# Performance work log

Measured on AMD Instinct MI355X. Metric: run time of the kernel, lower is better.

## Reference

```python
import jax, jax.numpy as jnp
import numpy as np

# Dims: B=16 graphs, T=354 timesteps (l_max), N=64 nodes, H=128 model dim, NS=32 complex SSM modes

def setup_inputs() -> dict:
    key = jax.random.key(0)
    ks = jax.random.split(key, 10)
    B, T, N, H, NS = 16, 354, 64, 128, 32
    x = jax.random.normal(ks[0], (B, T, N), jnp.float32)
    W_in = jax.random.normal(ks[1], (H, 1), jnp.float32) * 0.5
    b_in = jnp.zeros((H,), jnp.float32)
    # S4D params: timescales log-uniform in [1e-3, 1e-1], A = -1/2 + i*pi*n (S4D-Lin init)
    log_dt = (jnp.log(0.001) + jax.random.uniform(ks[2], (H,), jnp.float32) * (jnp.log(0.1) - jnp.log(0.001))).astype(jnp.float32)
    A_re = -0.5 * jnp.ones((H, NS), jnp.float32)
    A_im = jnp.broadcast_to(np.pi * jnp.arange(NS, dtype=jnp.float32), (H, NS)).astype(jnp.float32) + 0.0
    C_re = jax.random.normal(ks[3], (H, NS), jnp.float32) * (0.5 ** 0.5)
    C_im = jax.random.normal(ks[4], (H, NS), jnp.float32) * (0.5 ** 0.5)
    D = jax.random.normal(ks[5], (H,), jnp.float32)
    W_out = jax.random.normal(ks[6], (2 * H, H), jnp.float32) * (1.0 / np.sqrt(H))
    b_out = jnp.zeros((2 * H,), jnp.float32)
    W_cls = jax.random.normal(ks[7], (1, H), jnp.float32) * (1.0 / np.sqrt(H))
    b_cls = jnp.zeros((1,), jnp.float32)
    return {"x": x, "W_in": W_in, "b_in": b_in, "log_dt": log_dt, "A_re": A_re, "A_im": A_im,
            "C_re": C_re, "C_im": C_im, "D": D, "W_out": W_out, "b_out": b_out,
            "W_cls": W_cls, "b_cls": b_cls}


def reference(x, W_in, b_in, log_dt, A_re, A_im, C_re, C_im, D, W_out, b_out, W_cls, b_cls):
    B, T, N = x.shape
    H = W_in.shape[0]
    # (B,T,N) -> (B*N, T, 1) per-node scalar series
    u = x.transpose(0, 2, 1).reshape(B * N, T, 1)
    u = u * W_in[:, 0] + b_in            # input_proj: (BN, T, H)
    u = u.transpose(0, 2, 1)             # transposed layout: (BN, H, L)
    # ---- S4D kernel (ZOH discretization, conjugate-pair 2*Re trick) ----
    dt = jnp.exp(log_dt)                 # (H,)
    A = A_re + 1j * A_im                 # (H, NS) complex64
    dtA = A * dt[:, None]                # (H, NS)
    C = C_re + 1j * C_im
    C_disc = C * (jnp.exp(dtA) - 1.0) / A
    l = jnp.arange(T)
    vand = jnp.exp(dtA[:, :, None] * l)  # Vandermonde (H, NS, L)
    K = 2.0 * jnp.real(jnp.einsum('hn,hnl->hl', C_disc, vand))  # (H, L)
    # ---- FFT causal long convolution + skip ----
    n_fft = 2 * T
    yf = jnp.fft.rfft(u, n_fft) * jnp.fft.rfft(K, n_fft)
    y = jnp.fft.irfft(yf, n_fft)[..., :T] + D[:, None] * u   # (BN, H, L)
    y = jax.nn.gelu(y)
    # dropout: identity at inference
    # ---- position-wise output linear H -> 2H, then GLU over channels ----
    g = jnp.einsum('bhl,gh->bgl', y, W_out) + b_out[:, None]  # (BN, 2H, L)
    z = g[:, :H] * jax.nn.sigmoid(g[:, H:])                    # (BN, H, L)
    # ---- pooling + classifier ----
    node_feats = z.mean(axis=-1).reshape(B, N, H)
    graph_feats = node_feats.mean(axis=1)                      # (B, H)
    logits = graph_feats @ W_cls.T + b_cls                     # (B, 1)
    return logits
```

## Files before the change

### kernel.cpp

```cpp
#include <hip/hip_runtime.h>
#include <hip/hip_bf16.h>


#define B_  16
#define T_  354
#define N_  64
#define H_  128
#define NS_ 32
#define BN_ (B_*N_)
#define TP_ 384
#define KW_ 512
#define PAD_ 136
#define GC_ 4
#define NGC_ ((T_ + GC_ - 1) / GC_)
#define GT_ 16
#define NGT_ ((T_ + GT_ - 1) / GT_)
#define WB_ ((2 * H_ * H_) / 512)

typedef __attribute__((ext_vector_type(8))) short bf16x8;
typedef __attribute__((ext_vector_type(4))) float f32x4;

static __device__ __forceinline__ unsigned short f32_to_bf16(float f) {
    unsigned int u = __float_as_uint(f);
    unsigned int r = 0x7FFFu + ((u >> 16) & 1u);
    return (unsigned short)((u + r) >> 16);
}

static __device__ __forceinline__ void gload_lds4(const void* g, void* l) {
    __builtin_amdgcn_global_load_lds(
        (const __attribute__((address_space(1))) unsigned int*)g,
        (__attribute__((address_space(3))) unsigned int*)l, 4, 0, 0);
}

static __device__ __forceinline__ float gelu_f(float v) {
    float v2 = v * v;
    float x  = v * fmaf(0.0713548162726f, v2, 1.5957691216057f);
    float sg = 1.0f / (1.0f + __expf(-x));
    return v * sg;
}

__global__ __launch_bounds__(512) void k_pre(
        const float* __restrict__ log_dt,
        const float* __restrict__ A_re, const float* __restrict__ A_im,
        const float* __restrict__ C_re, const float* __restrict__ C_im,
        const float* __restrict__ b_in, const float* __restrict__ D,
        const float* __restrict__ x, const float* __restrict__ W_out,
        unsigned short* __restrict__ Krev, float* __restrict__ koff,
        unsigned short* __restrict__ xbf, unsigned short* __restrict__ Wbf) {
    const int blk = blockIdx.x;
    const int tid = threadIdx.x;

    if (blk >= H_ + 96) {
        int id = (blk - H_ - 96) * 512 + tid;
        if (id < 2 * H_ * H_) Wbf[id] = f32_to_bf16(W_out[id]);
        return;
    }
    if (blk >= H_) {
        __shared__ float xt[64][68];
        int idx = blk - H_;
        int bt = idx / 6, tt = idx % 6;
        int r  = tid >> 3, fc = tid & 7;
        int t  = tt * 64 + r;
        float4 v0 = make_float4(0.f, 0.f, 0.f, 0.f), v1 = v0;
        if (t < T_) {
            const float* xp = x + ((size_t)bt * T_ + t) * N_ + fc * 8;
            v0 = *(const float4*)xp;
            v1 = *(const float4*)(xp + 4);
        }
        *(float4*)&xt[r][fc * 8]     = v0;
        *(float4*)&xt[r][fc * 8 + 4] = v1;
        __syncthreads();
        int n = tid >> 3, tc = tid & 7;
        unsigned short pk[8];
#pragma unroll
        for (int k = 0; k < 8; k++) pk[k] = f32_to_bf16(xt[tc * 8 + k][n]);
        *(uint4*)(xbf + (size_t)(bt * 64 + n) * TP_ + tt * 64 + tc * 8)
            = *(const uint4*)pk;
        return;
    }

    const int h = blk;
    const int l = tid;
    float val = 0.0f;
    if (l < T_) {
        float dt = expf(log_dt[h]);
        float fl = (float)l;
#pragma unroll 4
        for (int m = 0; m < NS_; m++) {
            float are = A_re[h * NS_ + m], aim = A_im[h * NS_ + m];
            float dre = are * dt, dim = aim * dt;
            float er  = expf(dre);
            float c1, s1; __sincosf(dim, &s1, &c1);
            float e_re = er * c1, e_im = er * s1;
            float m_re = e_re - 1.0f, m_im = e_im;
            float inv  = 1.0f / (are * are + aim * aim);
            float q_re = (m_re * are + m_im * aim) * inv;
            float q_im = (m_im * are - m_re * aim) * inv;
            float c_r = C_re[h * NS_ + m], c_i = C_im[h * NS_ + m];
            float cdre = c_r * q_re - c_i * q_im;
            float cdim = c_r * q_im + c_i * q_re;
            float el = expf(dre * fl);
            float cl, sl; __sincosf(dim * fl, &sl, &cl);
            val += el * (cdre * cl - cdim * sl);
        }
        val *= 2.0f;
        if (l == 0) val += D[h];
    }

    __shared__ float sc[512];
    sc[l] = (l < T_) ? val : 0.0f;
    __syncthreads();
    for (int off = 1; off < 512; off <<= 1) {
        float add = (l >= off) ? sc[l - off] : 0.0f;
        __syncthreads();
        sc[l] += add;
        __syncthreads();
    }

    if (l < T_) {
        koff[l * H_ + h] = b_in[h] * sc[l];
        unsigned short bv = f32_to_bf16(val);
#pragma unroll
        for (int r = 0; r < 8; r++)
            Krev[((size_t)r * H_ + h) * KW_ + (T_ - 1 - l) + r] = bv;
    }
}

__global__ __launch_bounds__(256, 3) void k_conv(
        const unsigned short* __restrict__ xbf,
        const unsigned short* __restrict__ Krev,
        const float* __restrict__ koff,
        const float* __restrict__ W_in,
        unsigned short* __restrict__ Y) {
    __shared__ unsigned short x_lds[64 * PAD_];
    __shared__ unsigned short k_lds[128 * PAD_];

    const int tid  = threadIdx.x;
    const int w    = tid >> 6;
    const int lane = tid & 63;
    const int q    = lane >> 4;
    const int l16  = lane & 15;
    const int bn0  = blockIdx.x * 64;
    const int tg0  = blockIdx.y * GC_;

    float win[2][4];
#pragma unroll
    for (int mt = 0; mt < 2; mt++)
#pragma unroll
        for (int rr = 0; rr < 4; rr++)
            win[mt][rr] = W_in[32 * w + 16 * mt + 4 * q + rr];

    for (int g = 0; g < GC_; g++) {
        const int t = tg0 + g;
        if (t >= T_) break;
        const int nkb = (t >> 7) + 1;

        float ko[2][4];
#pragma unroll
        for (int mt = 0; mt < 2; mt++)
#pragma unroll
            for (int rr = 0; rr < 4; rr++)
                ko[mt][rr] = koff[t * H_ + 32 * w + 16 * mt + 4 * q + rr];

        f32x4 cacc[2][4];
#pragma unroll
        for (int mt = 0; mt < 2; mt++)
#pragma unroll
            for (int nt = 0; nt < 4; nt++) cacc[mt][nt] = (f32x4){0.f, 0.f, 0.f, 0.f};

        for (int kb = 0; kb < nkb; kb++) {
            const int tau0 = kb << 7;
            const int L    = 353 - t + tau0;
            const int cp   = (-L) & 7;
            const int kshi = min(3, (t - tau0) >> 5);
            __syncthreads();
#pragma unroll
            for (int i = 0; i < 16; i++) {
                int r = w * 16 + i;
                gload_lds4(xbf + (size_t)(bn0 + r) * TP_ + tau0 + lane * 2,
                           &x_lds[r * PAD_]);
            }
#pragma unroll 8
            for (int i = 0; i < 32; i++) {
                int hr = w * 32 + i;
                gload_lds4(Krev + ((size_t)cp * H_ + hr) * KW_ + (L + cp) + lane * 2,
                           &k_lds[hr * PAD_]);
            }
            __syncthreads();

            for (int ks = 0; ks <= kshi; ks++) {
                bf16x8 af[2], bf[4];
#pragma unroll
                for (int mt = 0; mt < 2; mt++)
                    af[mt] = *(const bf16x8*)&k_lds[(32 * w + 16 * mt + l16) * PAD_ + ks * 32 + q * 8];
#pragma unroll
                for (int nt = 0; nt < 4; nt++)
                    bf[nt] = *(const bf16x8*)&x_lds[(16 * nt + l16) * PAD_ + ks * 32 + q * 8];
#pragma unroll
                for (int mt = 0; mt < 2; mt++)
#pragma unroll
                    for (int nt = 0; nt < 4; nt++)
                        cacc[mt][nt] = __builtin_amdgcn_mfma_f32_16x16x32_bf16(
                            af[mt], bf[nt], cacc[mt][nt], 0, 0, 0);
            }
        }

        __syncthreads();
#pragma unroll
        for (int mt = 0; mt < 2; mt++)
#pragma unroll
            for (int nt = 0; nt < 4; nt++) {
                unsigned short pk[4];
#pragma unroll
                for (int rr = 0; rr < 4; rr++) {
                    float v = fmaf(cacc[mt][nt][rr], win[mt][rr], ko[mt][rr]);
                    pk[rr] = f32_to_bf16(gelu_f(v));
                }
                *(uint2*)&x_lds[(16 * nt + l16) * PAD_ + 32 * w + 16 * mt + 4 * q]
                    = *(const uint2*)pk;
            }
        __syncthreads();

#pragma unroll
        for (int i = 0; i < 4; i++) {
            int c    = i * 256 + tid;
            int row  = c >> 4;
            int col8 = (c & 15) * 8;
            uint4 v = *(const uint4*)&x_lds[row * PAD_ + col8];
            *(uint4*)(Y + ((size_t)t * BN_ + bn0 + row) * H_ + col8) = v;
        }
    }
}

__global__ __launch_bounds__(256, 4) void k_glu(
        const unsigned short* __restrict__ Y,
        const unsigned short* __restrict__ Wbf,
        const float* __restrict__ b_out,
        float* __restrict__ node_sum) {
    __shared__ unsigned short Yt[64 * PAD_];

    const int tid  = threadIdx.x;
    const int w    = tid >> 6;
    const int lane = tid & 63;
    const int q    = lane >> 4;
    const int l16  = lane & 15;
    const int jg   = blockIdx.x & 1;
    const int bn0  = (blockIdx.x >> 1) * 64;
    const int tg0  = blockIdx.y * GT_;
    const int jlow = jg * 64 + w * 16;
    const int jhigh = jlow + 128;

    bf16x8 wfrag[2][4];
#pragma unroll
    for (int ks = 0; ks < 4; ks++) {
        wfrag[0][ks] = *(const bf16x8*)(Wbf + (size_t)(jlow  + l16) * H_ + ks * 32 + q * 8);
        wfrag[1][ks] = *(const bf16x8*)(Wbf + (size_t)(jhigh + l16) * H_ + ks * 32 + q * 8);
    }
    float bo1[4], bo2[4];
#pragma unroll
    for (int rr = 0; rr < 4; rr++) {
        bo1[rr] = b_out[jlow  + 4 * q + rr];
        bo2[rr] = b_out[jhigh + 4 * q + rr];
    }

    f32x4 zacc[4];
#pragma unroll
    for (int nt = 0; nt < 4; nt++) zacc[nt] = (f32x4){0.f, 0.f, 0.f, 0.f};

    for (int g = 0; g < GT_; g++) {
        const int t = tg0 + g;
        if (t >= T_) break;
        __syncthreads();
#pragma unroll
        for (int i = 0; i < 16; i++) {
            int r = w * 16 + i;
            gload_lds4(Y + ((size_t)t * BN_ + bn0 + r) * H_ + lane * 2,
                       &Yt[r * PAD_]);
        }
        __syncthreads();

        f32x4 gacc[2][4];
#pragma unroll
        for (int mt = 0; mt < 2; mt++)
#pragma unroll
            for (int nt = 0; nt < 4; nt++) gacc[mt][nt] = (f32x4){0.f, 0.f, 0.f, 0.f};

#pragma unroll
        for (int ks = 0; ks < 4; ks++) {
            bf16x8 yf[4];
#pragma unroll
            for (int nt = 0; nt < 4; nt++)
                yf[nt] = *(const bf16x8*)&Yt[(16 * nt + l16) * PAD_ + ks * 32 + q * 8];
#pragma unroll
            for (int mt = 0; mt < 2; mt++)
#pragma unroll
                for (int nt = 0; nt < 4; nt++)
                    gacc[mt][nt] = __builtin_amdgcn_mfma_f32_16x16x32_bf16(
                        wfrag[mt][ks], yf[nt], gacc[mt][nt], 0, 0, 0);
        }

#pragma unroll
        for (int nt = 0; nt < 4; nt++)
#pragma unroll
            for (int rr = 0; rr < 4; rr++) {
                float a  = gacc[0][nt][rr] + bo1[rr];
                float bs = gacc[1][nt][rr] + bo2[rr];
                float sg = 1.0f / (1.0f + __expf(-bs));
                zacc[nt][rr] += a * sg;
            }
    }

#pragma unroll
    for (int nt = 0; nt < 4; nt++)
#pragma unroll
        for (int rr = 0; rr < 4; rr++) {
            int bn = bn0 + 16 * nt + l16;
            int j  = jlow + 4 * q + rr;
            atomicAdd(&node_sum[bn * H_ + j], zacc[nt][rr]);
        }
}

__global__ void k_cls(const float* __restrict__ node_sum,
                      const float* __restrict__ W_cls, const float* __restrict__ b_cls,
                      float* __restrict__ out) {
    const int b = blockIdx.x, tid = threadIdx.x;
    float s = 0.0f;
    for (int i = tid; i < N_ * H_; i += 256)
        s += node_sum[b * (N_ * H_) + i] * W_cls[i & (H_ - 1)];
    __shared__ float red[256];
    red[tid] = s;
    __syncthreads();
    for (int off = 128; off > 0; off >>= 1) {
        if (tid < off) red[tid] += red[tid + off];
        __syncthreads();
    }
    if (tid == 0) out[b] = red[0] * (1.0f / (354.0f * 64.0f)) + b_cls[0];
}

extern "C" void kernel_launch(void* const* d_in, const int* in_sizes, int n_in,
                              void* d_out, int out_size, void* d_ws, size_t ws_size,
                              hipStream_t stream) {
    const float* x      = (const float*)d_in[0];
    const float* W_in   = (const float*)d_in[1];
    const float* b_in   = (const float*)d_in[2];
    const float* log_dt = (const float*)d_in[3];
    const float* A_re   = (const float*)d_in[4];
    const float* A_im   = (const float*)d_in[5];
    const float* C_re   = (const float*)d_in[6];
    const float* C_im   = (const float*)d_in[7];
    const float* D      = (const float*)d_in[8];
    const float* W_out  = (const float*)d_in[9];
    const float* b_out  = (const float*)d_in[10];
    const float* W_cls  = (const float*)d_in[11];
    const float* b_cls  = (const float*)d_in[12];

    char* ws = (char*)d_ws;
    float*          node_sum = (float*)(ws + 0);
    unsigned short* Krev     = (unsigned short*)(ws + 524288);
    float*          koff     = (float*)(ws + 1572864);
    unsigned short* xbf      = (unsigned short*)(ws + 1754112);
    unsigned short* Wbf      = (unsigned short*)(ws + 2540544);
    unsigned short* Y        = (unsigned short*)(ws + 2606080);

    hipMemsetAsync(ws, 0, 1572864, stream);
    k_pre<<<dim3(H_ + 96 + WB_), dim3(512), 0, stream>>>(
        log_dt, A_re, A_im, C_re, C_im, b_in, D, x, W_out, Krev, koff, xbf, Wbf);
    k_conv<<<dim3(BN_ / 64, NGC_), dim3(256), 0, stream>>>(
        xbf, Krev, koff, W_in, Y);
    k_glu<<<dim3(2 * BN_ / 64, NGT_), dim3(256), 0, stream>>>(
        Y, Wbf, b_out, node_sum);
    k_cls<<<dim3(B_), dim3(256), 0, stream>>>(node_sum, W_cls, b_cls, (float*)d_out);
}
```

Baseline: 243.9 us.

## Register-prefetch software pipelining in conv and GLU kernels, halve GLU time grouping

Replaces the direct global-to-LDS loads in k_conv and k_glu with 16-byte register loads that prefetch the next tile while the current one is computed, then store it into LDS. k_glu gets a double-buffered LDS tile, and its time-group size drops from 16 to 8, giving more blocks. k_conv now writes its GELU outputs straight to global memory instead of staging them through LDS for coalescing. This aims to hide global load latency behind MFMA work. In exchange it raises register pressure, makes the Y stores less coalesced, and adds more atomic adds in k_glu because there are more blocks.

```diff
diff --git a/kernel.cpp b/kernel.cpp
--- a/kernel.cpp
+++ b/kernel.cpp
@@ -13,7 +13,7 @@
 #define PAD_ 136
 #define GC_ 4
 #define NGC_ ((T_ + GC_ - 1) / GC_)
-#define GT_ 16
+#define GT_ 8
 #define NGT_ ((T_ + GT_ - 1) / GT_)
 #define WB_ ((2 * H_ * H_) / 512)
 
@@ -24,12 +24,6 @@
     unsigned int u = __float_as_uint(f);
     unsigned int r = 0x7FFFu + ((u >> 16) & 1u);
     return (unsigned short)((u + r) >> 16);
-}
-
-static __device__ __forceinline__ void gload_lds4(const void* g, void* l) {
-    __builtin_amdgcn_global_load_lds(
-        (const __attribute__((address_space(1))) unsigned int*)g,
-        (__attribute__((address_space(3))) unsigned int*)l, 4, 0, 0);
 }
 
 static __device__ __forceinline__ float gelu_f(float v) {
@@ -135,13 +129,15 @@
     __shared__ unsigned short x_lds[64 * PAD_];
     __shared__ unsigned short k_lds[128 * PAD_];
 
-    const int tid  = threadIdx.x;
-    const int w    = tid >> 6;
-    const int lane = tid & 63;
-    const int q    = lane >> 4;
-    const int l16  = lane & 15;
-    const int bn0  = blockIdx.x * 64;
-    const int tg0  = blockIdx.y * GC_;
+    const int tid   = threadIdx.x;
+    const int w     = tid >> 6;
+    const int lane  = tid & 63;
+    const int q     = lane >> 4;
+    const int l16   = lane & 15;
+    const int bn0   = blockIdx.x * 64;
+    const int tg0   = blockIdx.y * GC_;
+    const int srow4 = lane >> 4;
+    const int scol  = l16 * 8;
 
     float win[2][4];
 #pragma unroll
@@ -150,85 +146,95 @@
         for (int rr = 0; rr < 4; rr++)
             win[mt][rr] = W_in[32 * w + 16 * mt + 4 * q + rr];
 
-    for (int g = 0; g < GC_; g++) {
-        const int t = tg0 + g;
-        if (t >= T_) break;
-        const int nkb = (t >> 7) + 1;
-
-        float ko[2][4];
-#pragma unroll
-        for (int mt = 0; mt < 2; mt++)
-#pragma unroll
-            for (int rr = 0; rr < 4; rr++)
-                ko[mt][rr] = koff[t * H_ + 32 * w + 16 * mt + 4 * q + rr];
-
-        f32x4 cacc[2][4];
-#pragma unroll
-        for (int mt = 0; mt < 2; mt++)
-#pragma unroll
-            for (int nt = 0; nt < 4; nt++) cacc[mt][nt] = (f32x4){0.f, 0.f, 0.f, 0.f};
-
-        for (int kb = 0; kb < nkb; kb++) {
-            const int tau0 = kb << 7;
-            const int L    = 353 - t + tau0;
-            const int cp   = (-L) & 7;
-            const int kshi = min(3, (t - tau0) >> 5);
-            __syncthreads();
-#pragma unroll
-            for (int i = 0; i < 16; i++) {
-                int r = w * 16 + i;
-                gload_lds4(xbf + (size_t)(bn0 + r) * TP_ + tau0 + lane * 2,
-                           &x_lds[r * PAD_]);
+    uint4 xr[4], kr[8];
+
+    auto LOAD = [&](int t, int kb) {
+        const int tau0 = kb << 7;
+        const int L    = 353 - t + tau0;
+        const int cp   = (-L) & 7;
+        const unsigned short* kbase = Krev + (size_t)cp * H_ * KW_ + (L + cp);
+#pragma unroll
+        for (int i = 0; i < 4; i++) {
+            int r = w * 16 + i * 4 + srow4;
+            xr[i] = *(const uint4*)(xbf + (size_t)(bn0 + r) * TP_ + tau0 + scol);
+        }
+#pragma unroll
+        for (int i = 0; i < 8; i++) {
+            int hr = w * 32 + i * 4 + srow4;
+            kr[i] = *(const uint4*)(kbase + (size_t)hr * KW_ + scol);
+        }
+    };
+    auto WRITE = [&]() {
+#pragma unroll
+        for (int i = 0; i < 4; i++) {
+            int r = w * 16 + i * 4 + srow4;
+            *(uint4*)&x_lds[r * PAD_ + scol] = xr[i];
+        }
+#pragma unroll
+        for (int i = 0; i < 8; i++) {
+            int hr = w * 32 + i * 4 + srow4;
+            *(uint4*)&k_lds[hr * PAD_ + scol] = kr[i];
+        }
+    };
+
+    f32x4 cacc[2][4];
+#pragma unroll
+    for (int mt = 0; mt < 2; mt++)
+#pragma unroll
+        for (int nt = 0; nt < 4; nt++) cacc[mt][nt] = (f32x4){0.f, 0.f, 0.f, 0.f};
+
+    int t = tg0, kb = 0;
+    bool valid = true;
+    LOAD(t, kb);
+    while (valid) {
+        int tn = t, kbn = kb + 1;
+        if (kbn > (t >> 7)) { tn = t + 1; kbn = 0; }
+        bool vn = (tn < T_) && (tn < tg0 + GC_);
+
+        __syncthreads();
+        WRITE();
+        if (vn) LOAD(tn, kbn);
+        __syncthreads();
+
+        const int tau0 = kb << 7;
+        const int kshi = min(3, (t - tau0) >> 5);
+        for (int ks = 0; ks <= kshi; ks++) {
+            bf16x8 af[2], bf[4];
+#pragma unroll
+            for (int mt = 0; mt < 2; mt++)
+                af[mt] = *(const bf16x8*)&k_lds[(32 * w + 16 * mt + l16) * PAD_ + ks * 32 + q * 8];
+#pragma unroll
+            for (int nt = 0; nt < 4; nt++)
+                bf[nt] = *(const bf16x8*)&x_lds[(16 * nt + l16) * PAD_ + ks * 32 + q * 8];
+#pragma unroll
+            for (int mt = 0; mt < 2; mt++)
+#pragma unroll
+                for (int nt = 0; nt < 4; nt++)
+                    cacc[mt][nt] = __builtin_amdgcn_mfma_f32_16x16x32_bf16(
+                        af[mt], bf[nt], cacc[mt][nt], 0, 0, 0);
+        }
+
+        if (kb == (t >> 7)) {
+#pragma unroll
+            for (int mt = 0; mt < 2; mt++) {
+                int h0 = 32 * w + 16 * mt + 4 * q;
+#pragma unroll
+                for (int nt = 0; nt < 4; nt++) {
+                    unsigned short pk[4];
+#pragma unroll
+                    for (int rr = 0; rr < 4; rr++) {
+                        float v = fmaf(cacc[mt][nt][rr], win[mt][rr],
+                                       koff[t * H_ + h0 + rr]);
+                        pk[rr] = f32_to_bf16(gelu_f(v));
+                    }
+                    int bn = bn0 + 16 * nt + l16;
+                    *(uint2*)(Y + ((size_t)t * BN_ + bn) * H_ + h0)
+                        = *(const uint2*)pk;
+                    cacc[mt][nt] = (f32x4){0.f, 0.f, 0.f, 0.f};
+                }
             }
-#pragma unroll 8
-            for (int i = 0; i < 32; i++) {
-                int hr = w * 32 + i;
-                gload_lds4(Krev + ((size_t)cp * H_ + hr) * KW_ + (L + cp) + lane * 2,
-                           &k_lds[hr * PAD_]);
-            }
-            __syncthreads();
-
-            for (int ks = 0; ks <= kshi; ks++) {
-                bf16x8 af[2], bf[4];
-#pragma unroll
-                for (int mt = 0; mt < 2; mt++)
-                    af[mt] = *(const bf16x8*)&k_lds[(32 * w + 16 * mt + l16) * PAD_ + ks * 32 + q * 8];
-#pragma unroll
-                for (int nt = 0; nt < 4; nt++)
-                    bf[nt] = *(const bf16x8*)&x_lds[(16 * nt + l16) * PAD_ + ks * 32 + q * 8];
-#pragma unroll
-                for (int mt = 0; mt < 2; mt++)
-#pragma unroll
-                    for (int nt = 0; nt < 4; nt++)
-                        cacc[mt][nt] = __builtin_amdgcn_mfma_f32_16x16x32_bf16(
-                            af[mt], bf[nt], cacc[mt][nt], 0, 0, 0);
-            }
-        }
-
-        __syncthreads();
-#pragma unroll
-        for (int mt = 0; mt < 2; mt++)
-#pragma unroll
-            for (int nt = 0; nt < 4; nt++) {
-                unsigned short pk[4];
-#pragma unroll
-                for (int rr = 0; rr < 4; rr++) {
-                    float v = fmaf(cacc[mt][nt][rr], win[mt][rr], ko[mt][rr]);
-                    pk[rr] = f32_to_bf16(gelu_f(v));
-                }
-                *(uint2*)&x_lds[(16 * nt + l16) * PAD_ + 32 * w + 16 * mt + 4 * q]
-                    = *(const uint2*)pk;
-            }
-        __syncthreads();
-
-#pragma unroll
-        for (int i = 0; i < 4; i++) {
-            int c    = i * 256 + tid;
-            int row  = c >> 4;
-            int col8 = (c & 15) * 8;
-            uint4 v = *(const uint4*)&x_lds[row * PAD_ + col8];
-            *(uint4*)(Y + ((size_t)t * BN_ + bn0 + row) * H_ + col8) = v;
-        }
+        }
+        t = tn; kb = kbn; valid = vn;
     }
 }
 
@@ -237,18 +243,20 @@
         const unsigned short* __restrict__ Wbf,
         const float* __restrict__ b_out,
         float* __restrict__ node_sum) {
-    __shared__ unsigned short Yt[64 * PAD_];
-
-    const int tid  = threadIdx.x;
-    const int w    = tid >> 6;
-    const int lane = tid & 63;
-    const int q    = lane >> 4;
-    const int l16  = lane & 15;
-    const int jg   = blockIdx.x & 1;
-    const int bn0  = (blockIdx.x >> 1) * 64;
-    const int tg0  = blockIdx.y * GT_;
-    const int jlow = jg * 64 + w * 16;
+    __shared__ unsigned short Yt[2][64 * PAD_];
+
+    const int tid   = threadIdx.x;
+    const int w     = tid >> 6;
+    const int lane  = tid & 63;
+    const int q     = lane >> 4;
+    const int l16   = lane & 15;
+    const int jg    = blockIdx.x & 1;
+    const int bn0   = (blockIdx.x >> 1) * 64;
+    const int tg0   = blockIdx.y * GT_;
+    const int jlow  = jg * 64 + w * 16;
     const int jhigh = jlow + 128;
+    const int srow4 = lane >> 4;
+    const int scol  = l16 * 8;
 
     bf16x8 wfrag[2][4];
 #pragma unroll
@@ -263,21 +271,35 @@
         bo2[rr] = b_out[jhigh + 4 * q + rr];
     }
 
+    uint4 pre[4];
+    auto LOADT = [&](int t) {
+#pragma unroll
+        for (int i = 0; i < 4; i++) {
+            int r = w * 16 + i * 4 + srow4;
+            pre[i] = *(const uint4*)(Y + ((size_t)t * BN_ + bn0 + r) * H_ + scol);
+        }
+    };
+    auto WRITEB = [&](int b) {
+#pragma unroll
+        for (int i = 0; i < 4; i++) {
+            int r = w * 16 + i * 4 + srow4;
+            *(uint4*)&Yt[b][r * PAD_ + scol] = pre[i];
+        }
+    };
+
     f32x4 zacc[4];
 #pragma unroll
     for (int nt = 0; nt < 4; nt++) zacc[nt] = (f32x4){0.f, 0.f, 0.f, 0.f};
+
+    LOADT(tg0);
+    WRITEB(0);
+    __syncthreads();
 
     for (int g = 0; g < GT_; g++) {
         const int t = tg0 + g;
         if (t >= T_) break;
-        __syncthreads();
-#pragma unroll
-        for (int i = 0; i < 16; i++) {
-            int r = w * 16 + i;
-            gload_lds4(Y + ((size_t)t * BN_ + bn0 + r) * H_ + lane * 2,
-                       &Yt[r * PAD_]);
-        }
-        __syncthreads();
+        const bool hn = (g + 1 < GT_) && (t + 1 < T_);
+        if (hn) LOADT(t + 1);
 
         f32x4 gacc[2][4];
 #pragma unroll
@@ -285,12 +307,13 @@
 #pragma unroll
             for (int nt = 0; nt < 4; nt++) gacc[mt][nt] = (f32x4){0.f, 0.f, 0.f, 0.f};
 
+        const unsigned short* buf = Yt[g & 1];
 #pragma unroll
         for (int ks = 0; ks < 4; ks++) {
             bf16x8 yf[4];
 #pragma unroll
             for (int nt = 0; nt < 4; nt++)
-                yf[nt] = *(const bf16x8*)&Yt[(16 * nt + l16) * PAD_ + ks * 32 + q * 8];
+                yf[nt] = *(const bf16x8*)&buf[(16 * nt + l16) * PAD_ + ks * 32 + q * 8];
 #pragma unroll
             for (int mt = 0; mt < 2; mt++)
 #pragma unroll
@@ -308,6 +331,9 @@
                 float sg = 1.0f / (1.0f + __expf(-bs));
                 zacc[nt][rr] += a * sg;
             }
+
+        if (hn) WRITEB((g + 1) & 1);
+        __syncthreads();
     }
 
 #pragma unroll
```

New measurement: 406.5 us. 66.7% more time.

## Compute two timesteps per conv block sharing x tiles, load K directly to registers

Applied to the files above, without the earlier changes.

The conv kernel now handles two adjacent output timesteps per block, so each loaded x tile in LDS feeds both timesteps' MFMAs. The K operand is read straight from global memory into registers instead of being staged through a separate LDS buffer, which frees LDS and removes that copy. The causal k-substep skipping (kshi) is dropped, so each active block step runs all four k-substeps. The grid grows to T/2 blocks in y, and the GLU kernel's time tile shrinks from 16 to 8. Costs are more accumulator registers and uncoalesced-per-lane global loads for K.

```diff
diff --git a/kernel.cpp b/kernel.cpp
--- a/kernel.cpp
+++ b/kernel.cpp
@@ -11,9 +11,7 @@
 #define TP_ 384
 #define KW_ 512
 #define PAD_ 136
-#define GC_ 4
-#define NGC_ ((T_ + GC_ - 1) / GC_)
-#define GT_ 16
+#define GT_ 8
 #define NGT_ ((T_ + GT_ - 1) / GT_)
 #define WB_ ((2 * H_ * H_) / 512)
 
@@ -133,7 +131,6 @@
         const float* __restrict__ W_in,
         unsigned short* __restrict__ Y) {
     __shared__ unsigned short x_lds[64 * PAD_];
-    __shared__ unsigned short k_lds[128 * PAD_];
 
     const int tid  = threadIdx.x;
     const int w    = tid >> 6;
@@ -141,7 +138,8 @@
     const int q    = lane >> 4;
     const int l16  = lane & 15;
     const int bn0  = blockIdx.x * 64;
-    const int tg0  = blockIdx.y * GC_;
+    const int t0   = blockIdx.y * 2;
+    const int nkb  = ((t0 + 1) >> 7) + 1;
 
     float win[2][4];
 #pragma unroll
@@ -150,49 +148,45 @@
         for (int rr = 0; rr < 4; rr++)
             win[mt][rr] = W_in[32 * w + 16 * mt + 4 * q + rr];
 
-    for (int g = 0; g < GC_; g++) {
-        const int t = tg0 + g;
-        if (t >= T_) break;
-        const int nkb = (t >> 7) + 1;
-
-        float ko[2][4];
+    f32x4 cacc[2][2][4];
+#pragma unroll
+    for (int tt = 0; tt < 2; tt++)
 #pragma unroll
         for (int mt = 0; mt < 2; mt++)
 #pragma unroll
-            for (int rr = 0; rr < 4; rr++)
-                ko[mt][rr] = koff[t * H_ + 32 * w + 16 * mt + 4 * q + rr];
-
-        f32x4 cacc[2][4];
-#pragma unroll
-        for (int mt = 0; mt < 2; mt++)
-#pragma unroll
-            for (int nt = 0; nt < 4; nt++) cacc[mt][nt] = (f32x4){0.f, 0.f, 0.f, 0.f};
-
-        for (int kb = 0; kb < nkb; kb++) {
-            const int tau0 = kb << 7;
-            const int L    = 353 - t + tau0;
-            const int cp   = (-L) & 7;
-            const int kshi = min(3, (t - tau0) >> 5);
-            __syncthreads();
-#pragma unroll
-            for (int i = 0; i < 16; i++) {
-                int r = w * 16 + i;
-                gload_lds4(xbf + (size_t)(bn0 + r) * TP_ + tau0 + lane * 2,
-                           &x_lds[r * PAD_]);
-            }
-#pragma unroll 8
-            for (int i = 0; i < 32; i++) {
-                int hr = w * 32 + i;
-                gload_lds4(Krev + ((size_t)cp * H_ + hr) * KW_ + (L + cp) + lane * 2,
-                           &k_lds[hr * PAD_]);
-            }
-            __syncthreads();
-
-            for (int ks = 0; ks <= kshi; ks++) {
-                bf16x8 af[2], bf[4];
+            for (int nt = 0; nt < 4; nt++)
+                cacc[tt][mt][nt] = (f32x4){0.f, 0.f, 0.f, 0.f};
+
+    for (int kb = 0; kb < nkb; kb++) {
+        const int tau0 = kb << 7;
+        __syncthreads();
+#pragma unroll
+        for (int i = 0; i < 16; i++) {
+            int r = w * 16 + i;
+            gload_lds4(xbf + (size_t)(bn0 + r) * TP_ + tau0 + lane * 2,
+                       &x_lds[r * PAD_]);
+        }
+        __syncthreads();
+
+#pragma unroll
+        for (int tt = 0; tt < 2; tt++) {
+            const int t = t0 + tt;
+            if (tau0 > t) continue;
+            const int L  = 353 - t + tau0;
+            const int cp = (-L) & 7;
+            const unsigned short* kbase = Krev + (size_t)cp * H_ * KW_ + (L + cp);
+
+            bf16x8 kf[4][2];
+#pragma unroll
+            for (int ks = 0; ks < 4; ks++)
 #pragma unroll
                 for (int mt = 0; mt < 2; mt++)
-                    af[mt] = *(const bf16x8*)&k_lds[(32 * w + 16 * mt + l16) * PAD_ + ks * 32 + q * 8];
+                    kf[ks][mt] = *(const bf16x8*)(kbase
+                        + (size_t)(32 * w + 16 * mt + l16) * KW_ + ks * 32 + q * 8);
+
+#pragma unroll
+            for (int ks = 0; ks < 4; ks++) {
+                bf16x8 bf[4];
 #pragma unroll
                 for (int nt = 0; nt < 4; nt++)
                     bf[nt] = *(const bf16x8*)&x_lds[(16 * nt + l16) * PAD_ + ks * 32 + q * 8];
@@ -200,27 +194,32 @@
                 for (int mt = 0; mt < 2; mt++)
 #pragma unroll
                     for (int nt = 0; nt < 4; nt++)
-                        cacc[mt][nt] = __builtin_amdgcn_mfma_f32_16x16x32_bf16(
-                            af[mt], bf[nt], cacc[mt][nt], 0, 0, 0);
+                        cacc[tt][mt][nt] = __builtin_amdgcn_mfma_f32_16x16x32_bf16(
+                            kf[ks][mt], bf[nt], cacc[tt][mt][nt], 0, 0, 0);
             }
         }
-
-        __syncthreads();
-#pragma unroll
-        for (int mt = 0; mt < 2; mt++)
+    }
+
+#pragma unroll
+    for (int tt = 0; tt < 2; tt++) {
+        const int t = t0 + tt;
+        __syncthreads();
+#pragma unroll
+        for (int mt = 0; mt < 2; mt++) {
+            int h0 = 32 * w + 16 * mt + 4 * q;
 #pragma unroll
             for (int nt = 0; nt < 4; nt++) {
                 unsigned short pk[4];
 #pragma unroll
                 for (int rr = 0; rr < 4; rr++) {
-                    float v = fmaf(cacc[mt][nt][rr], win[mt][rr], ko[mt][rr]);
+                    float v = fmaf(cacc[tt][mt][nt][rr], win[mt][rr],
+                                   koff[t * H_ + h0 + rr]);
                     pk[rr] = f32_to_bf16(gelu_f(v));
                 }
-                *(uint2*)&x_lds[(16 * nt + l16) * PAD_ + 32 * w + 16 * mt + 4 * q]
-                    = *(const uint2*)pk;
+                *(uint2*)&x_lds[(16 * nt + l16) * PAD_ + h0] = *(const uint2*)pk;
             }
-        __syncthreads();
-
+        }
+        __syncthreads();
 #pragma unroll
         for (int i = 0; i < 4; i++) {
             int c    = i * 256 + tid;
@@ -365,7 +364,7 @@
     hipMemsetAsync(ws, 0, 1572864, stream);
     k_pre<<<dim3(H_ + 96 + WB_), dim3(512), 0, stream>>>(
         log_dt, A_re, A_im, C_re, C_im, b_in, D, x, W_out, Krev, koff, xbf, Wbf);
-    k_conv<<<dim3(BN_ / 64, NGC_), dim3(256), 0, stream>>>(
+    k_conv<<<dim3(BN_ / 64, T_ / 2), dim3(256), 0, stream>>>(
         xbf, Krev, koff, W_in, Y);
     k_glu<<<dim3(2 * BN_ / 64, NGT_), dim3(256), 0, stream>>>(
         Y, Wbf, b_out, node_sum);
```

After: 281.3 us. 1.15x slower.
